# Optimization experiments

Measured on AMD Instinct MI355X. Metric: run time of the kernel, lower is better.

## Reference

```python
import jax, jax.numpy as jnp
import numpy as np

DIM = 512; NHEAD = 8; DHEAD = 64; INNER = NHEAD * DHEAD
CTX = 1024; NOCT = int(np.ceil(np.log2(CTX))) + 1  # 11
B = 8; SEQ = 256; MEM = 768


def positional_encoding(ctx, num_oct):
    # matches Attention.positional_encoding on coords=arange(ctx).view(ctx,1),
    # start_octave = 1 - num_oct
    coords = jnp.arange(ctx, dtype=jnp.float32)[:, None, None]        # (ctx,1,1)
    octaves = jnp.arange(1 - num_oct, 1, dtype=jnp.float32)           # (num_oct,)
    mult = (2.0 ** octaves) * np.pi
    scaled = (coords * mult).reshape(ctx, num_oct)                    # (ctx, num_oct)
    return jnp.concatenate([jnp.sin(scaled), jnp.cos(scaled)], axis=-1)  # (ctx, 2*num_oct)


def get_shifts(mem, seq, ctx):
    coords = jnp.arange(mem + seq - 1, -1, -1) - (seq - 1)            # (mem+seq,)
    shifts = coords[None, :] + jnp.arange(seq)[:, None]               # (seq, mem+seq)
    oob = (shifts < 0) | (shifts > ctx - 1)
    bias = jnp.where(oob, -jnp.inf, 0.0).astype(jnp.float32)
    return jnp.clip(shifts, 0, ctx - 1), bias


def setup_inputs() -> dict:
    key = jax.random.key(0)
    ks = jax.random.split(key, 8)
    s = 0.02
    return {
        "x": jax.random.normal(ks[0], (B, SEQ, DIM), jnp.float32),
        "memory": jax.random.normal(ks[1], (B, MEM, DIM), jnp.float32),
        "W_qkv": jax.random.normal(ks[2], (DIM, 3 * INNER), jnp.float32) * s,
        "W_rel": jax.random.normal(ks[3], (2 * NOCT, INNER), jnp.float32) * s,
        "W_out": jax.random.normal(ks[4], (INNER, DIM), jnp.float32) * s,
        "b_out": jnp.zeros((DIM,), jnp.float32),
        "u_emb": jax.random.normal(ks[5], (DHEAD,), jnp.float32),
        "v_emb": jax.random.normal(ks[6], (DHEAD,), jnp.float32),
    }


def reference(x, memory, W_qkv, W_rel, W_out, b_out, u_emb, v_emb):
    b, seq, _ = x.shape
    mem = memory.shape[1]
    total = mem + seq
    scale = DHEAD ** -0.5

    shifts, bias = get_shifts(mem, seq, CTX)                          # (seq,total) each
    R = positional_encoding(CTX, NOCT)                                # (CTX, 2*NOCT)
    kr = (R @ W_rel)[shifts].reshape(seq, total, NHEAD, DHEAD)        # n m h d

    qkv = jnp.concatenate([memory, x], axis=1) @ W_qkv                # (b,total,3*INNER)
    q, k, v = jnp.split(qkv, 3, axis=-1)

    def heads(t):
        return t.reshape(b, total, NHEAD, DHEAD).transpose(0, 2, 1, 3)  # b h m d

    q = heads(q)[:, :, mem:]                                          # b h n d (queries only over x)
    k = heads(k)
    v = heads(v)

    term_a = jnp.einsum('bhnd,bhmd->bhnm', q, k)
    term_b = jnp.einsum('bhnd,nmhd->bhnm', q, kr)
    term_c = jnp.einsum('d,bhmd->bhm', u_emb, k)[:, :, None, :]        # broadcast over n
    term_d = jnp.einsum('d,nmhd->hnm', v_emb, kr)[None]                # broadcast over b

    dots = (term_a + term_b + term_c + term_d) * scale + bias          # banded -inf mask
    attn = jax.nn.softmax(dots, axis=-1)                               # dropout p=0 -> identity
    out = jnp.einsum('bhnm,bhmd->bnhd', attn, v).reshape(b, seq, INNER)
    return out @ W_out + b_out
```

## Files before the change

### kernel.cpp

```cpp
#include <hip/hip_runtime.h>
#include <hip/hip_bf16.h>
#include <math.h>

typedef unsigned short u16;
typedef unsigned int u32;
typedef __attribute__((ext_vector_type(8))) short short8;
typedef __attribute__((ext_vector_type(4))) float floatx4;

constexpr int kB     = 8;
constexpr int kSEQ   = 256;
constexpr int kMEM   = 768;
constexpr int kTOTAL = 1024;

__device__ __forceinline__ float bf2f(u16 u) {
  return __uint_as_float(((u32)u) << 16);
}
__device__ __forceinline__ u16 f2bf(float f) {
  __hip_bfloat16 h = __float2bfloat16(f);
  return *reinterpret_cast<u16*>(&h);
}
__device__ __forceinline__ void gload_lds16(const u16* g, u16* l) {
  __builtin_amdgcn_global_load_lds(
      (__attribute__((address_space(1))) const unsigned int*)g,
      (__attribute__((address_space(3))) unsigned int*)l, 16, 0, 0);
}

__global__ __launch_bounds__(256) void rrel_kernel(
    const float* __restrict__ W_rel, const float* __restrict__ v_emb,
    u16* __restrict__ Rrel_bf, float* __restrict__ vR)
{
  __shared__ float pe[22];
  __shared__ float prod[512];
  int s = blockIdx.x;
  int t = threadIdx.x;
  if (t < 22) {
    int o = (t < 11) ? t : (t - 11);
    float mult = ldexpf(3.14159265358979323846f, o - 10);
    float ang = (float)s * mult;
    pe[t] = (t < 11) ? sinf(ang) : cosf(ang);
  }
  __syncthreads();
#pragma unroll
  for (int c = 0; c < 2; c++) {
    int j = t + c * 256;
    float acc = 0.f;
#pragma unroll
    for (int o = 0; o < 22; ++o) acc += pe[o] * W_rel[o * 512 + j];
    Rrel_bf[(size_t)s * 512 + j] = f2bf(acc);
    prod[j] = acc * v_emb[j & 63];
  }
  __syncthreads();
  if (t < 8) {
    float a = 0.f;
#pragma unroll 8
    for (int d = 0; d < 64; d++) a += prod[t * 64 + d];
    vR[t * 1024 + s] = a * 0.125f;
  }
}

__device__ __forceinline__ void wtconv_body(
    const float* __restrict__ W, u16* __restrict__ Wt, int K, int N,
    int n0, int k0, int tid, float (*tile)[65])
{
  int r = tid >> 4, c4 = (tid & 15) * 4;
#pragma unroll
  for (int v = 0; v < 4; v++) {
    float4 w4 = *(const float4*)(W + (size_t)(k0 + v * 16 + r) * N + n0 + c4);
    tile[v * 16 + r][c4 + 0] = w4.x;
    tile[v * 16 + r][c4 + 1] = w4.y;
    tile[v * 16 + r][c4 + 2] = w4.z;
    tile[v * 16 + r][c4 + 3] = w4.w;
  }
  __syncthreads();
#pragma unroll
  for (int v = 0; v < 4; v++) {
    int rn = v * 16 + r;
    ushort4 o;
    o.x = f2bf(tile[c4 + 0][rn]);
    o.y = f2bf(tile[c4 + 1][rn]);
    o.z = f2bf(tile[c4 + 2][rn]);
    o.w = f2bf(tile[c4 + 3][rn]);
    *(ushort4*)(Wt + (size_t)(n0 + rn) * K + k0 + c4) = o;
  }
}

__global__ __launch_bounds__(256) void xw_kernel(
    const float* __restrict__ x, const float* __restrict__ memf,
    const float* __restrict__ W_qkv, const float* __restrict__ W_out,
    u16* __restrict__ Xb, u16* __restrict__ WqkvT, u16* __restrict__ WoutT)
{
  __shared__ float tile[64][65];
  int bid = blockIdx.x;
  int tid = threadIdx.x;
  if (bid < 2048) {
    int idx = bid * 256 + tid;
    int row = idx >> 6, c8 = idx & 63;
    int b = row >> 10, pos = row & 1023;
    const float* src = (pos < kMEM)
        ? memf + (size_t)(b * kMEM + pos) * 512
        : x    + (size_t)(b * kSEQ + pos - kMEM) * 512;
    const float4* s4 = (const float4*)(src + c8 * 8);
    float4 a = s4[0], bb = s4[1];
    u16 tmp[8] = {f2bf(a.x),  f2bf(a.y),  f2bf(a.z),  f2bf(a.w),
                  f2bf(bb.x), f2bf(bb.y), f2bf(bb.z), f2bf(bb.w)};
    *(uint4*)(Xb + (size_t)row * 512 + c8 * 8) = *(uint4*)tmp;
  } else if (bid < 2240) {
    int r = bid - 2048;
    wtconv_body(W_qkv, WqkvT, 512, 1536, (r % 24) * 64, (r / 24) * 64, tid, tile);
  } else {
    int r = bid - 2240;
    wtconv_body(W_out, WoutT, 512, 512, (r % 8) * 64, (r / 8) * 64, tid, tile);
  }
}

__global__ __launch_bounds__(256) void gemm_bf16(
    const u16* __restrict__ A, const u16* __restrict__ Bt,
    int lda, int ldb, int ksteps,
    u16* __restrict__ Cbf, float* __restrict__ Cf, int ldc,
    const float* __restrict__ colAdd, int mode)
{
  __shared__ u16 As[128 * 64];
  __shared__ u16 Bs[128 * 64];
  int tid = threadIdx.x;
  int id = blockIdx.y * gridDim.x + blockIdx.x;
  int gy = gridDim.y;
  int bm = (id % gy) * 128, bn = (id / gy) * 128;
  int ln = tid & 15, quad = (tid >> 4) & 3, w = tid >> 6;
  int moff = (w >> 1) * 64, noff = (w & 1) * 64;
  int l7 = ln & 7;
  floatx4 acc[4][4];
#pragma unroll
  for (int mi = 0; mi < 4; mi++)
#pragma unroll
    for (int ni = 0; ni < 4; ni++) acc[mi][ni] = (floatx4){0.f, 0.f, 0.f, 0.f};

  int srow[4], sgch[4];
#pragma unroll
  for (int v = 0; v < 4; v++) {
    int f = v * 256 + tid;
    srow[v] = f >> 3;
    sgch[v] = (f & 7) ^ ((f >> 3) & 7);
  }

  for (int ks = 0; ks < ksteps; ks++) {
    int k0 = ks * 64;
#pragma unroll
    for (int v = 0; v < 4; v++) {
      gload_lds16(A + (size_t)(bm + srow[v]) * lda + k0 + sgch[v] * 8,
                  &As[(v * 256 + tid) * 8]);
      gload_lds16(Bt + (size_t)(bn + srow[v]) * ldb + k0 + sgch[v] * 8,
                  &Bs[(v * 256 + tid) * 8]);
    }
    __syncthreads();
#pragma unroll
    for (int kb = 0; kb < 2; kb++) {
      short8 af[4], bfr[4];
#pragma unroll
      for (int mi = 0; mi < 4; mi++) {
        int row = moff + mi * 16 + ln;
        af[mi] = *(const short8*)&As[row * 64 + (((quad + 4 * kb) ^ l7) << 3)];
      }
#pragma unroll
      for (int ni = 0; ni < 4; ni++) {
        int row = noff + ni * 16 + ln;
        bfr[ni] = *(const short8*)&Bs[row * 64 + (((quad + 4 * kb) ^ l7) << 3)];
      }
#pragma unroll
      for (int mi = 0; mi < 4; mi++)
#pragma unroll
        for (int ni = 0; ni < 4; ni++)
          acc[mi][ni] = __builtin_amdgcn_mfma_f32_16x16x32_bf16(
              af[mi], bfr[ni], acc[mi][ni], 0, 0, 0);
    }
    __syncthreads();
  }

  int r0 = bm + moff + quad * 4;
#pragma unroll
  for (int ni = 0; ni < 4; ni++) {
    int col = bn + noff + ni * 16 + ln;
    float cv = (mode == 2) ? colAdd[col] : 0.f;
    float scale = (mode == 0 && col < 512) ? 0.125f : 1.f;
#pragma unroll
    for (int mi = 0; mi < 4; mi++) {
#pragma unroll
      for (int r = 0; r < 4; r++) {
        int row = r0 + mi * 16 + r;
        float val = acc[mi][ni][r];
        if (mode == 2) Cf[(size_t)row * ldc + col] = val + cv;
        else           Cbf[(size_t)row * ldc + col] = f2bf(val * scale);
      }
    }
  }
}

__global__ __launch_bounds__(256) void uk_kernel(
    const u16* __restrict__ qkv_bf, const float* __restrict__ u_emb,
    float* __restrict__ uk)
{
  int idx = blockIdx.x * 256 + threadIdx.x;
  int b = idx >> 13, h = (idx >> 10) & 7, m = idx & 1023;
  const u16* kp = qkv_bf + (size_t)(b * kTOTAL + m) * 1536 + 512 + h * 64;
  const float4* ue4 = (const float4*)u_emb;
  float acc = 0.f;
#pragma unroll
  for (int c = 0; c < 8; c++) {
    uint4 raw = *(const uint4*)(kp + c * 8);
    const u16* us = (const u16*)&raw;
    float4 ua = ue4[2 * c], ub = ue4[2 * c + 1];
    acc += bf2f(us[0]) * ua.x + bf2f(us[1]) * ua.y + bf2f(us[2]) * ua.z + bf2f(us[3]) * ua.w
         + bf2f(us[4]) * ub.x + bf2f(us[5]) * ub.y + bf2f(us[6]) * ub.z + bf2f(us[7]) * ub.w;
  }
  uk[idx] = acc * 0.125f;
}

__global__ __launch_bounds__(256) void attn_mfma(
    const u16* __restrict__ qkv_bf, const u16* __restrict__ Rrel_bf,
    const float* __restrict__ vR, const float* __restrict__ uk,
    u16* __restrict__ Opart, float* __restrict__ lbuf)
{
  constexpr int LD  = 72;
  constexpr int TLD = 84;
  __shared__ u16 Vt[64 * LD];
  __shared__ u16 Ps[64 * LD];
  __shared__ u16 Tl[4 * 16 * TLD];

  int nt = blockIdx.x >> 3, p = blockIdx.x & 7;
  int h = blockIdx.y, b = blockIdx.z;
  int n0 = nt * 64, bh = b * 8 + h;
  int tid = threadIdx.x;
  int w = tid >> 6, lane = tid & 63;
  int l15 = lane & 15, quad = lane >> 4, q8 = quad * 8;

  int sr0 = tid >> 3, sc8 = tid & 7;
  int sr1 = (256 + tid) >> 3;
  int vg0 = ((sr0 >> 3) ^ sc8) * 8 + (sr0 & 7);
  int vg1 = ((sr1 >> 3) ^ sc8) * 8 + (sr1 & 7);

  const u16* qrow = qkv_bf + (size_t)(b * kTOTAL + kMEM + n0 + 16 * w + l15) * 1536 + h * 64;
  short8 qf0 = *(const short8*)(qrow + q8);
  short8 qf1 = *(const short8*)(qrow + 32 + q8);

  const u16* kpart = qkv_bf + (size_t)(b * kTOTAL) * 1536 + 512 + h * 64;
  const float* ukrow = uk + (size_t)bh * 1024 + l15;
  const float* vRh = vR + h * 1024;
  u16* Tw = Tl + w * 16 * TLD;

  floatx4 o_acc[4];
  float l_i[4];
#pragma unroll
  for (int r = 0; r < 4; r++) l_i[r] = 0.f;
#pragma unroll
  for (int nd = 0; nd < 4; nd++) o_acc[nd] = (floatx4){0.f, 0.f, 0.f, 0.f};

  int s_base_w = kMEM + n0 + 16 * w;
  int ntiles = 13 + nt;
  for (int mt = p; mt < ntiles; mt += 8) {
    int m0 = mt * 64;
    const u16* kbase = kpart + (size_t)m0 * 1536;
    int sb = s_base_w - m0;

    uint4 vreg0 = *(const uint4*)(kbase + 512 + (size_t)sr0 * 1536 + sc8 * 8);
    uint4 vreg1 = *(const uint4*)(kbase + 512 + (size_t)sr1 * 1536 + sc8 * 8);
    short8 kb0[4], kb1[4];
#pragma unroll
    for (int ni = 0; ni < 4; ni++) {
      const u16* kr = kbase + (size_t)(16 * ni + l15) * 1536;
      kb0[ni] = *(const short8*)(kr + q8);
      kb1[ni] = *(const short8*)(kr + 32 + q8);
    }
    short8 rb0[5], rb1[5];
    float vRc[5];
#pragma unroll
    for (int ct = 0; ct < 5; ct++) {
      int s = sb - 63 + 16 * ct + l15;
      s = min(max(s, 0), 1023);
      const u16* rr = Rrel_bf + (size_t)s * 512 + h * 64;
      rb0[ct] = *(const short8*)(rr + q8);
      rb1[ct] = *(const short8*)(rr + 32 + q8);
      vRc[ct] = vRh[s];
    }
    float ukc[4];
#pragma unroll
    for (int ni = 0; ni < 4; ni++) ukc[ni] = ukrow[m0 + ni * 16];

    __syncthreads();
    {
      const u16* vp0 = (const u16*)&vreg0;
      const u16* vp1 = (const u16*)&vreg1;
#pragma unroll
      for (int i = 0; i < 8; i++) {
        Vt[(sc8 * 8 + i) * LD + vg0] = vp0[i];
        Vt[(sc8 * 8 + i) * LD + vg1] = vp1[i];
      }
    }
    __syncthreads();

#pragma unroll
    for (int ct = 0; ct < 5; ct++) {
      floatx4 t = (floatx4){0.f, 0.f, 0.f, 0.f};
      t = __builtin_amdgcn_mfma_f32_16x16x32_bf16(qf0, rb0[ct], t, 0, 0, 0);
      t = __builtin_amdgcn_mfma_f32_16x16x32_bf16(qf1, rb1[ct], t, 0, 0, 0);
#pragma unroll
      for (int r = 0; r < 4; r++)
        Tw[(4 * quad + r) * TLD + 16 * ct + l15] = f2bf(t[r] + vRc[ct]);
    }

    floatx4 s_acc[4];
#pragma unroll
    for (int ni = 0; ni < 4; ni++) {
      floatx4 sa = (floatx4){0.f, 0.f, 0.f, 0.f};
      sa = __builtin_amdgcn_mfma_f32_16x16x32_bf16(qf0, kb0[ni], sa, 0, 0, 0);
      sa = __builtin_amdgcn_mfma_f32_16x16x32_bf16(qf1, kb1[ni], sa, 0, 0, 0);
      s_acc[ni] = sa;
    }

    bool lastt = (mt == ntiles - 1);
#pragma unroll
    for (int r = 0; r < 4; r++) {
      int il = 4 * quad + r;
      float ls = 0.f;
      float pv[4];
#pragma unroll
      for (int ni = 0; ni < 4; ni++) {
        float tsh = bf2f(Tw[il * TLD + 63 + il - 16 * ni - l15]);
        float val = s_acc[ni][r] + tsh + ukc[ni];
        if (lastt && (16 * ni + l15) > (16 * w + il)) val = -1e30f;
        float e = __expf(val);
        pv[ni] = e;
        ls += e;
      }
      l_i[r] += ls;
      int prow = 16 * w + il;
      int rr3p = prow >> 3;
      int base = prow * LD + (l15 & 7);
#pragma unroll
      for (int ni = 0; ni < 4; ni++)
        Ps[base + (((2 * ni + (l15 >> 3)) ^ rr3p) << 3)] = f2bf(pv[ni]);
    }

    int rowq = 16 * w + l15, rr3q = rowq >> 3;
    short8 pa0 = *(const short8*)&Ps[rowq * LD + ((quad ^ rr3q) << 3)];
    short8 pa1 = *(const short8*)&Ps[rowq * LD + (((quad + 4) ^ rr3q) << 3)];
#pragma unroll
    for (int nd = 0; nd < 4; nd++) {
      int rowv = 16 * nd + l15, rr3v = rowv >> 3;
      short8 vb0 = *(const short8*)&Vt[rowv * LD + ((quad ^ rr3v) << 3)];
      short8 vb1 = *(const short8*)&Vt[rowv * LD + (((quad + 4) ^ rr3v) << 3)];
      o_acc[nd] = __builtin_amdgcn_mfma_f32_16x16x32_bf16(pa0, vb0, o_acc[nd], 0, 0, 0);
      o_acc[nd] = __builtin_amdgcn_mfma_f32_16x16x32_bf16(pa1, vb1, o_acc[nd], 0, 0, 0);
    }
  }

  int pbase = (p * 64 + bh) * 256;
#pragma unroll
  for (int r = 0; r < 4; r++) {
    float l = l_i[r];
#pragma unroll
    for (int off = 1; off < 16; off <<= 1)
      l += __shfl_xor(l, off, 64);
    int n = n0 + 16 * w + 4 * quad + r;
    u16* orow = Opart + ((size_t)(pbase + n) << 6) + l15;
#pragma unroll
    for (int nd = 0; nd < 4; nd++)
      orow[16 * nd] = f2bf(o_acc[nd][r]);
    if (l15 == 0) lbuf[pbase + n] = l;
  }
}

__global__ __launch_bounds__(256) void attn_combine(
    const u16* __restrict__ Opart, const float* __restrict__ lbuf,
    u16* __restrict__ aout_bf)
{
  int idx = blockIdx.x * 256 + threadIdx.x;
  int bh = idx >> 12, n = (idx >> 4) & 255, d4 = idx & 15;
  int rowi = bh * 256 + n;
  float den = 0.f;
  float num[4] = {0.f, 0.f, 0.f, 0.f};
#pragma unroll
  for (int p = 0; p < 8; p++) {
    den += lbuf[(p << 14) + rowi];
    uint2 raw = *(const uint2*)(Opart + (((size_t)(p << 14) + rowi) << 6) + d4 * 4);
    const u16* us = (const u16*)&raw;
#pragma unroll
    for (int j = 0; j < 4; j++) num[j] += bf2f(us[j]);
  }
  float inv = 1.f / den;
  int b = bh >> 3, h = bh & 7;
  ushort4 o;
  o.x = f2bf(num[0] * inv);
  o.y = f2bf(num[1] * inv);
  o.z = f2bf(num[2] * inv);
  o.w = f2bf(num[3] * inv);
  *(ushort4*)(aout_bf + (size_t)(b * kSEQ + n) * 512 + h * 64 + d4 * 4) = o;
}

extern "C" void kernel_launch(void* const* d_in, const int* in_sizes, int n_in,
                              void* d_out, int out_size, void* d_ws, size_t ws_size,
                              hipStream_t stream) {
  (void)in_sizes; (void)n_in; (void)out_size; (void)ws_size;
  const float* x      = (const float*)d_in[0];
  const float* memory = (const float*)d_in[1];
  const float* W_qkv  = (const float*)d_in[2];
  const float* W_rel  = (const float*)d_in[3];
  const float* W_out  = (const float*)d_in[4];
  const float* b_out  = (const float*)d_in[5];
  const float* u_emb  = (const float*)d_in[6];
  const float* v_emb  = (const float*)d_in[7];
  float* out = (float*)d_out;

  char* ws = (char*)d_ws;
  u16*   qkv_bf  = (u16*)ws;                         ws += (size_t)12582912 * 2;
  u16*   Xcat_bf = (u16*)ws;                         ws += (size_t)4194304 * 2;
  u16*   aout_bf = (u16*)ws;                         ws += (size_t)1048576 * 2;
  u16*   Opart   = (u16*)ws;                         ws += (size_t)8388608 * 2;
  float* lbuf    = (float*)ws;                       ws += (size_t)131072 * 4;
  u16*   WqkvT   = (u16*)ws;                         ws += (size_t)786432 * 2;
  u16*   WoutT   = (u16*)ws;                         ws += (size_t)262144 * 2;
  u16*   Rrel_bf = (u16*)ws;                         ws += (size_t)524288 * 2;
  float* vR      = (float*)ws;                       ws += (size_t)8192 * 4;
  float* uk      = (float*)ws;                       ws += (size_t)65536 * 4;

  rrel_kernel<<<1024, 256, 0, stream>>>(W_rel, v_emb, Rrel_bf, vR);
  xw_kernel<<<2304, 256, 0, stream>>>(x, memory, W_qkv, W_out, Xcat_bf, WqkvT, WoutT);

  gemm_bf16<<<dim3(12, 64), 256, 0, stream>>>(
      Xcat_bf, WqkvT, 512, 512, 8, qkv_bf, nullptr, 1536, nullptr, 0);

  uk_kernel<<<256, 256, 0, stream>>>(qkv_bf, u_emb, uk);

  attn_mfma<<<dim3(32, 8, 8), 256, 0, stream>>>(qkv_bf, Rrel_bf, vR, uk, Opart, lbuf);
  attn_combine<<<1024, 256, 0, stream>>>(Opart, lbuf, aout_bf);

  gemm_bf16<<<dim3(4, 16), 256, 0, stream>>>(
      aout_bf, WoutT, 512, 512, 8, nullptr, out, 512, b_out, 2);
}
```

Measured before the change: 174.7 us.

## Precompute relative-position bias via batched GEMM and pre-transposed V

Computes the q·R_rel positional term (plus v·R and u·k biases) for every query and relative shift up front with a batched GEMM, scattered into a per-(b,h) skewed bias matrix qB in bf16. A new kernel writes a transposed V copy alongside the u·k reduction. The attention kernel then just reads these bias values and the V^T fragments from global memory, dropping its per-tile R_rel MFMAs, LDS V transpose, skew buffer and two barriers. This adds a large intermediate buffer and extra global traffic, and the bias is now summed before bf16 rounding, which changes numerics slightly.

```diff
diff --git a/kernel.cpp b/kernel.cpp
--- a/kernel.cpp
+++ b/kernel.cpp
@@ -116,12 +116,17 @@
 __global__ __launch_bounds__(256) void gemm_bf16(
     const u16* __restrict__ A, const u16* __restrict__ Bt,
     int lda, int ldb, int ksteps,
-    u16* __restrict__ Cbf, float* __restrict__ Cf, int ldc,
-    const float* __restrict__ colAdd, int mode)
+    long long aStrideB, int aStrideH, int bStrideH,
+    u16* __restrict__ Cbf, float* __restrict__ Cf, int ldc, long long cStrideZ,
+    const float* __restrict__ colAdd, int colAddStrideH,
+    const float* __restrict__ ukp, int mode)
 {
   __shared__ u16 As[128 * 64];
   __shared__ u16 Bs[128 * 64];
   int tid = threadIdx.x;
+  int z = blockIdx.z;
+  const u16* Ab = A + (size_t)(z >> 3) * aStrideB + (size_t)(z & 7) * aStrideH;
+  const u16* Bb = Bt + (size_t)(z & 7) * bStrideH;
   int id = blockIdx.y * gridDim.x + blockIdx.x;
   int gy = gridDim.y;
   int bm = (id % gy) * 128, bn = (id / gy) * 128;
@@ -146,9 +151,9 @@
     int k0 = ks * 64;
 #pragma unroll
     for (int v = 0; v < 4; v++) {
-      gload_lds16(A + (size_t)(bm + srow[v]) * lda + k0 + sgch[v] * 8,
+      gload_lds16(Ab + (size_t)(bm + srow[v]) * lda + k0 + sgch[v] * 8,
                   &As[(v * 256 + tid) * 8]);
-      gload_lds16(Bt + (size_t)(bn + srow[v]) * ldb + k0 + sgch[v] * 8,
+      gload_lds16(Bb + (size_t)(bn + srow[v]) * ldb + k0 + sgch[v] * 8,
                   &Bs[(v * 256 + tid) * 8]);
     }
     __syncthreads();
@@ -176,10 +181,12 @@
   }
 
   int r0 = bm + moff + quad * 4;
+  const float* vRp = (mode == 3) ? colAdd + (size_t)(z & 7) * colAddStrideH : colAdd;
+  const float* ukz = (mode == 3) ? ukp + (size_t)z * 1024 : nullptr;
 #pragma unroll
   for (int ni = 0; ni < 4; ni++) {
     int col = bn + noff + ni * 16 + ln;
-    float cv = (mode == 2) ? colAdd[col] : 0.f;
+    float cv = (mode == 2) ? colAdd[col] : (mode == 3 ? vRp[col] : 0.f);
     float scale = (mode == 0 && col < 512) ? 0.125f : 1.f;
 #pragma unroll
     for (int mi = 0; mi < 4; mi++) {
@@ -187,43 +194,73 @@
       for (int r = 0; r < 4; r++) {
         int row = r0 + mi * 16 + r;
         float val = acc[mi][ni][r];
-        if (mode == 2) Cf[(size_t)row * ldc + col] = val + cv;
-        else           Cbf[(size_t)row * ldc + col] = f2bf(val * scale);
+        if (mode == 2) {
+          Cf[(size_t)row * ldc + col] = val + cv;
+        } else if (mode == 3) {
+          int m = 768 + row - col;
+          if (m >= 0)
+            Cbf[cStrideZ * z + (size_t)row * 1024 + m] = f2bf(val + cv + ukz[m]);
+        } else {
+          Cbf[(size_t)row * ldc + col] = f2bf(val * scale);
+        }
       }
     }
   }
 }
 
-__global__ __launch_bounds__(256) void uk_kernel(
+__global__ __launch_bounds__(256) void ukvt_kernel(
     const u16* __restrict__ qkv_bf, const float* __restrict__ u_emb,
-    float* __restrict__ uk)
-{
-  int idx = blockIdx.x * 256 + threadIdx.x;
-  int b = idx >> 13, h = (idx >> 10) & 7, m = idx & 1023;
-  const u16* kp = qkv_bf + (size_t)(b * kTOTAL + m) * 1536 + 512 + h * 64;
-  const float4* ue4 = (const float4*)u_emb;
-  float acc = 0.f;
-#pragma unroll
-  for (int c = 0; c < 8; c++) {
-    uint4 raw = *(const uint4*)(kp + c * 8);
-    const u16* us = (const u16*)&raw;
-    float4 ua = ue4[2 * c], ub = ue4[2 * c + 1];
-    acc += bf2f(us[0]) * ua.x + bf2f(us[1]) * ua.y + bf2f(us[2]) * ua.z + bf2f(us[3]) * ua.w
-         + bf2f(us[4]) * ub.x + bf2f(us[5]) * ub.y + bf2f(us[6]) * ub.z + bf2f(us[7]) * ub.w;
-  }
-  uk[idx] = acc * 0.125f;
-}
-
-__global__ __launch_bounds__(256) void attn_mfma(
-    const u16* __restrict__ qkv_bf, const u16* __restrict__ Rrel_bf,
-    const float* __restrict__ vR, const float* __restrict__ uk,
-    u16* __restrict__ Opart, float* __restrict__ lbuf)
-{
-  constexpr int LD  = 72;
-  constexpr int TLD = 84;
-  __shared__ u16 Vt[64 * LD];
+    float* __restrict__ uk, u16* __restrict__ VT)
+{
+  __shared__ u16 vt[64 * 72];
+  __shared__ float kred[64 * 8];
+  int bh = blockIdx.x >> 4, mt = blockIdx.x & 15;
+  int b = bh >> 3, h = bh & 7, m0 = mt * 64;
+  int t = threadIdx.x;
+  int c8 = t & 7;
+  const u16* base = qkv_bf + (size_t)(b * kTOTAL + m0) * 1536 + 512 + h * 64 + c8 * 8;
+  float up[8];
+#pragma unroll
+  for (int i = 0; i < 8; i++) up[i] = u_emb[c8 * 8 + i];
+
+#pragma unroll
+  for (int v = 0; v < 2; v++) {
+    int row = (v * 256 + t) >> 3;
+    uint4 kv = *(const uint4*)(base + (size_t)row * 1536);
+    uint4 vv = *(const uint4*)(base + (size_t)row * 1536 + 512);
+    const u16* ku = (const u16*)&kv;
+    const u16* vu = (const u16*)&vv;
+    float s = 0.f;
+#pragma unroll
+    for (int i = 0; i < 8; i++) s += bf2f(ku[i]) * up[i];
+    kred[row * 8 + c8] = s;
+    int vg = (((row >> 3) ^ c8) << 3) + (row & 7);
+#pragma unroll
+    for (int i = 0; i < 8; i++) vt[(c8 * 8 + i) * 72 + vg] = vu[i];
+  }
+  __syncthreads();
+  if (t < 64) {
+    float a = 0.f;
+#pragma unroll
+    for (int i = 0; i < 8; i++) a += kred[t * 8 + i];
+    uk[(size_t)bh * 1024 + m0 + t] = a * 0.125f;
+  }
+#pragma unroll
+  for (int v = 0; v < 2; v++) {
+    int f = v * 256 + t;
+    int d = f >> 3, mc8 = f & 7;
+    uint4 o = *(const uint4*)&vt[d * 72 + (((mc8 ^ (d >> 3)) << 3))];
+    *(uint4*)(VT + ((size_t)(bh * 64 + d) << 10) + m0 + mc8 * 8) = o;
+  }
+}
+
+__global__ __launch_bounds__(256, 4) void attn_mfma(
+    const u16* __restrict__ qkv_bf, const u16* __restrict__ qB,
+    const u16* __restrict__ VT, u16* __restrict__ Opart,
+    float* __restrict__ lbuf)
+{
+  constexpr int LD = 72;
   __shared__ u16 Ps[64 * LD];
-  __shared__ u16 Tl[4 * 16 * TLD];
 
   int nt = blockIdx.x >> 3, p = blockIdx.x & 7;
   int h = blockIdx.y, b = blockIdx.z;
@@ -232,19 +269,13 @@
   int w = tid >> 6, lane = tid & 63;
   int l15 = lane & 15, quad = lane >> 4, q8 = quad * 8;
 
-  int sr0 = tid >> 3, sc8 = tid & 7;
-  int sr1 = (256 + tid) >> 3;
-  int vg0 = ((sr0 >> 3) ^ sc8) * 8 + (sr0 & 7);
-  int vg1 = ((sr1 >> 3) ^ sc8) * 8 + (sr1 & 7);
-
   const u16* qrow = qkv_bf + (size_t)(b * kTOTAL + kMEM + n0 + 16 * w + l15) * 1536 + h * 64;
   short8 qf0 = *(const short8*)(qrow + q8);
   short8 qf1 = *(const short8*)(qrow + 32 + q8);
 
   const u16* kpart = qkv_bf + (size_t)(b * kTOTAL) * 1536 + 512 + h * 64;
-  const float* ukrow = uk + (size_t)bh * 1024 + l15;
-  const float* vRh = vR + h * 1024;
-  u16* Tw = Tl + w * 16 * TLD;
+  const u16* vtbase = VT + ((size_t)(bh * 64) << 10);
+  const u16* qbrow = qB + ((size_t)bh << 18) + (size_t)(n0 + 16 * w + 4 * quad) * 1024 + l15;
 
   floatx4 o_acc[4];
   float l_i[4];
@@ -253,15 +284,11 @@
 #pragma unroll
   for (int nd = 0; nd < 4; nd++) o_acc[nd] = (floatx4){0.f, 0.f, 0.f, 0.f};
 
-  int s_base_w = kMEM + n0 + 16 * w;
   int ntiles = 13 + nt;
   for (int mt = p; mt < ntiles; mt += 8) {
     int m0 = mt * 64;
     const u16* kbase = kpart + (size_t)m0 * 1536;
-    int sb = s_base_w - m0;
-
-    uint4 vreg0 = *(const uint4*)(kbase + 512 + (size_t)sr0 * 1536 + sc8 * 8);
-    uint4 vreg1 = *(const uint4*)(kbase + 512 + (size_t)sr1 * 1536 + sc8 * 8);
+
     short8 kb0[4], kb1[4];
 #pragma unroll
     for (int ni = 0; ni < 4; ni++) {
@@ -269,42 +296,12 @@
       kb0[ni] = *(const short8*)(kr + q8);
       kb1[ni] = *(const short8*)(kr + 32 + q8);
     }
-    short8 rb0[5], rb1[5];
-    float vRc[5];
-#pragma unroll
-    for (int ct = 0; ct < 5; ct++) {
-      int s = sb - 63 + 16 * ct + l15;
-      s = min(max(s, 0), 1023);
-      const u16* rr = Rrel_bf + (size_t)s * 512 + h * 64;
-      rb0[ct] = *(const short8*)(rr + q8);
-      rb1[ct] = *(const short8*)(rr + 32 + q8);
-      vRc[ct] = vRh[s];
-    }
-    float ukc[4];
-#pragma unroll
-    for (int ni = 0; ni < 4; ni++) ukc[ni] = ukrow[m0 + ni * 16];
-
-    __syncthreads();
-    {
-      const u16* vp0 = (const u16*)&vreg0;
-      const u16* vp1 = (const u16*)&vreg1;
-#pragma unroll
-      for (int i = 0; i < 8; i++) {
-        Vt[(sc8 * 8 + i) * LD + vg0] = vp0[i];
-        Vt[(sc8 * 8 + i) * LD + vg1] = vp1[i];
-      }
-    }
-    __syncthreads();
-
-#pragma unroll
-    for (int ct = 0; ct < 5; ct++) {
-      floatx4 t = (floatx4){0.f, 0.f, 0.f, 0.f};
-      t = __builtin_amdgcn_mfma_f32_16x16x32_bf16(qf0, rb0[ct], t, 0, 0, 0);
-      t = __builtin_amdgcn_mfma_f32_16x16x32_bf16(qf1, rb1[ct], t, 0, 0, 0);
+    u16 qbu[4][4];
+#pragma unroll
+    for (int ni = 0; ni < 4; ni++)
 #pragma unroll
       for (int r = 0; r < 4; r++)
-        Tw[(4 * quad + r) * TLD + 16 * ct + l15] = f2bf(t[r] + vRc[ct]);
-    }
+        qbu[ni][r] = qbrow[(size_t)r * 1024 + m0 + 16 * ni];
 
     floatx4 s_acc[4];
 #pragma unroll
@@ -319,24 +316,19 @@
 #pragma unroll
     for (int r = 0; r < 4; r++) {
       int il = 4 * quad + r;
+      int prow = 16 * w + il;
       float ls = 0.f;
-      float pv[4];
+      int rr3p = prow >> 3;
+      int base = prow * LD + (l15 & 7);
 #pragma unroll
       for (int ni = 0; ni < 4; ni++) {
-        float tsh = bf2f(Tw[il * TLD + 63 + il - 16 * ni - l15]);
-        float val = s_acc[ni][r] + tsh + ukc[ni];
-        if (lastt && (16 * ni + l15) > (16 * w + il)) val = -1e30f;
+        float val = s_acc[ni][r] + bf2f(qbu[ni][r]);
+        if (lastt && (16 * ni + l15) > prow) val = -1e30f;
         float e = __expf(val);
-        pv[ni] = e;
         ls += e;
+        Ps[base + (((2 * ni + (l15 >> 3)) ^ rr3p) << 3)] = f2bf(e);
       }
       l_i[r] += ls;
-      int prow = 16 * w + il;
-      int rr3p = prow >> 3;
-      int base = prow * LD + (l15 & 7);
-#pragma unroll
-      for (int ni = 0; ni < 4; ni++)
-        Ps[base + (((2 * ni + (l15 >> 3)) ^ rr3p) << 3)] = f2bf(pv[ni]);
     }
 
     int rowq = 16 * w + l15, rr3q = rowq >> 3;
@@ -344,9 +336,9 @@
     short8 pa1 = *(const short8*)&Ps[rowq * LD + (((quad + 4) ^ rr3q) << 3)];
 #pragma unroll
     for (int nd = 0; nd < 4; nd++) {
-      int rowv = 16 * nd + l15, rr3v = rowv >> 3;
-      short8 vb0 = *(const short8*)&Vt[rowv * LD + ((quad ^ rr3v) << 3)];
-      short8 vb1 = *(const short8*)&Vt[rowv * LD + (((quad + 4) ^ rr3v) << 3)];
+      const u16* vr = vtbase + ((size_t)(16 * nd + l15) << 10) + m0;
+      short8 vb0 = *(const short8*)(vr + q8);
+      short8 vb1 = *(const short8*)(vr + 32 + q8);
       o_acc[nd] = __builtin_amdgcn_mfma_f32_16x16x32_bf16(pa0, vb0, o_acc[nd], 0, 0, 0);
       o_acc[nd] = __builtin_amdgcn_mfma_f32_16x16x32_bf16(pa1, vb1, o_acc[nd], 0, 0, 0);
     }
@@ -412,6 +404,8 @@
   char* ws = (char*)d_ws;
   u16*   qkv_bf  = (u16*)ws;                         ws += (size_t)12582912 * 2;
   u16*   Xcat_bf = (u16*)ws;                         ws += (size_t)4194304 * 2;
+  u16*   qB      = (u16*)ws;                         ws += (size_t)16777216 * 2;
+  u16*   VT      = (u16*)ws;                         ws += (size_t)4194304 * 2;
   u16*   aout_bf = (u16*)ws;                         ws += (size_t)1048576 * 2;
   u16*   Opart   = (u16*)ws;                         ws += (size_t)8388608 * 2;
   float* lbuf    = (float*)ws;                       ws += (size_t)131072 * 4;
@@ -424,14 +418,21 @@
   rrel_kernel<<<1024, 256, 0, stream>>>(W_rel, v_emb, Rrel_bf, vR);
   xw_kernel<<<2304, 256, 0, stream>>>(x, memory, W_qkv, W_out, Xcat_bf, WqkvT, WoutT);
 
-  gemm_bf16<<<dim3(12, 64), 256, 0, stream>>>(
-      Xcat_bf, WqkvT, 512, 512, 8, qkv_bf, nullptr, 1536, nullptr, 0);
-
-  uk_kernel<<<256, 256, 0, stream>>>(qkv_bf, u_emb, uk);
-
-  attn_mfma<<<dim3(32, 8, 8), 256, 0, stream>>>(qkv_bf, Rrel_bf, vR, uk, Opart, lbuf);
+  gemm_bf16<<<dim3(12, 64, 1), 256, 0, stream>>>(
+      Xcat_bf, WqkvT, 512, 512, 8, 0, 0, 0,
+      qkv_bf, nullptr, 1536, 0, nullptr, 0, nullptr, 0);
+
+  ukvt_kernel<<<1024, 256, 0, stream>>>(qkv_bf, u_emb, uk, VT);
+
+  gemm_bf16<<<dim3(8, 2, 64), 256, 0, stream>>>(
+      qkv_bf + (size_t)768 * 1536, Rrel_bf, 1536, 512, 1,
+      (long long)1024 * 1536, 64, 64,
+      qB, nullptr, 1024, 262144, vR, 1024, uk, 3);
+
+  attn_mfma<<<dim3(32, 8, 8), 256, 0, stream>>>(qkv_bf, qB, VT, Opart, lbuf);
   attn_combine<<<1024, 256, 0, stream>>>(Opart, lbuf, aout_bf);
 
-  gemm_bf16<<<dim3(4, 16), 256, 0, stream>>>(
-      aout_bf, WoutT, 512, 512, 8, nullptr, out, 512, b_out, 2);
-}
+  gemm_bf16<<<dim3(4, 16, 1), 256, 0, stream>>>(
+      aout_bf, WoutT, 512, 512, 8, 0, 0, 0,
+      nullptr, out, 512, 0, b_out, 0, nullptr, 2);
+}
```

New measurement: 203.8 us. 16.6% more time.

## Precompute relative-position scores with batched GEMM before attention

Applied to the files above, without the earlier changes.

Moves the q·R relative-position term (plus the v·R bias) out of the attention kernel into a separate batched bf16 GEMM. Each batch-head computes Q times all 1024 relative embeddings and scatters the result into a shifted (query, key) score buffer. The attention kernel then reads one precomputed bf16 value per score element instead of running extra MFMAs and an LDS shift per tile. In exchange it adds a 32 MB intermediate buffer that must be written and read back, which trades compute and LDS traffic for global memory bandwidth. The extra launch computes all 1024 relative positions, including ones the band later discards.

```diff
diff --git a/kernel.cpp b/kernel.cpp
--- a/kernel.cpp
+++ b/kernel.cpp
@@ -116,12 +116,16 @@
 __global__ __launch_bounds__(256) void gemm_bf16(
     const u16* __restrict__ A, const u16* __restrict__ Bt,
     int lda, int ldb, int ksteps,
-    u16* __restrict__ Cbf, float* __restrict__ Cf, int ldc,
-    const float* __restrict__ colAdd, int mode)
+    long long aStrideB, int aStrideH, int bStrideH,
+    u16* __restrict__ Cbf, float* __restrict__ Cf, int ldc, long long cStrideZ,
+    const float* __restrict__ colAdd, int colAddStrideH, int mode)
 {
   __shared__ u16 As[128 * 64];
   __shared__ u16 Bs[128 * 64];
   int tid = threadIdx.x;
+  int z = blockIdx.z;
+  const u16* Ab = A + (size_t)(z >> 3) * aStrideB + (size_t)(z & 7) * aStrideH;
+  const u16* Bb = Bt + (size_t)(z & 7) * bStrideH;
   int id = blockIdx.y * gridDim.x + blockIdx.x;
   int gy = gridDim.y;
   int bm = (id % gy) * 128, bn = (id / gy) * 128;
@@ -146,9 +150,9 @@
     int k0 = ks * 64;
 #pragma unroll
     for (int v = 0; v < 4; v++) {
-      gload_lds16(A + (size_t)(bm + srow[v]) * lda + k0 + sgch[v] * 8,
+      gload_lds16(Ab + (size_t)(bm + srow[v]) * lda + k0 + sgch[v] * 8,
                   &As[(v * 256 + tid) * 8]);
-      gload_lds16(Bt + (size_t)(bn + srow[v]) * ldb + k0 + sgch[v] * 8,
+      gload_lds16(Bb + (size_t)(bn + srow[v]) * ldb + k0 + sgch[v] * 8,
                   &Bs[(v * 256 + tid) * 8]);
     }
     __syncthreads();
@@ -176,10 +180,11 @@
   }
 
   int r0 = bm + moff + quad * 4;
+  const float* vRp = (mode == 3) ? colAdd + (size_t)(z & 7) * colAddStrideH : colAdd;
 #pragma unroll
   for (int ni = 0; ni < 4; ni++) {
     int col = bn + noff + ni * 16 + ln;
-    float cv = (mode == 2) ? colAdd[col] : 0.f;
+    float cv = (mode == 2) ? colAdd[col] : (mode == 3 ? vRp[col] : 0.f);
     float scale = (mode == 0 && col < 512) ? 0.125f : 1.f;
 #pragma unroll
     for (int mi = 0; mi < 4; mi++) {
@@ -187,8 +192,15 @@
       for (int r = 0; r < 4; r++) {
         int row = r0 + mi * 16 + r;
         float val = acc[mi][ni][r];
-        if (mode == 2) Cf[(size_t)row * ldc + col] = val + cv;
-        else           Cbf[(size_t)row * ldc + col] = f2bf(val * scale);
+        if (mode == 2) {
+          Cf[(size_t)row * ldc + col] = val + cv;
+        } else if (mode == 3) {
+          int m = 768 + row - col;
+          if (m >= 0)
+            Cbf[cStrideZ * z + (size_t)row * 1024 + m] = f2bf(val + cv);
+        } else {
+          Cbf[(size_t)row * ldc + col] = f2bf(val * scale);
+        }
       }
     }
   }
@@ -215,15 +227,13 @@
 }
 
 __global__ __launch_bounds__(256) void attn_mfma(
-    const u16* __restrict__ qkv_bf, const u16* __restrict__ Rrel_bf,
-    const float* __restrict__ vR, const float* __restrict__ uk,
-    u16* __restrict__ Opart, float* __restrict__ lbuf)
-{
-  constexpr int LD  = 72;
-  constexpr int TLD = 84;
+    const u16* __restrict__ qkv_bf, const u16* __restrict__ qB,
+    const float* __restrict__ uk, u16* __restrict__ Opart,
+    float* __restrict__ lbuf)
+{
+  constexpr int LD = 72;
   __shared__ u16 Vt[64 * LD];
   __shared__ u16 Ps[64 * LD];
-  __shared__ u16 Tl[4 * 16 * TLD];
 
   int nt = blockIdx.x >> 3, p = blockIdx.x & 7;
   int h = blockIdx.y, b = blockIdx.z;
@@ -242,9 +252,8 @@
   short8 qf1 = *(const short8*)(qrow + 32 + q8);
 
   const u16* kpart = qkv_bf + (size_t)(b * kTOTAL) * 1536 + 512 + h * 64;
+  const u16* qbrow = qB + ((size_t)bh << 18) + (size_t)(n0 + 16 * w + 4 * quad) * 1024 + l15;
   const float* ukrow = uk + (size_t)bh * 1024 + l15;
-  const float* vRh = vR + h * 1024;
-  u16* Tw = Tl + w * 16 * TLD;
 
   floatx4 o_acc[4];
   float l_i[4];
@@ -253,12 +262,10 @@
 #pragma unroll
   for (int nd = 0; nd < 4; nd++) o_acc[nd] = (floatx4){0.f, 0.f, 0.f, 0.f};
 
-  int s_base_w = kMEM + n0 + 16 * w;
   int ntiles = 13 + nt;
   for (int mt = p; mt < ntiles; mt += 8) {
     int m0 = mt * 64;
     const u16* kbase = kpart + (size_t)m0 * 1536;
-    int sb = s_base_w - m0;
 
     uint4 vreg0 = *(const uint4*)(kbase + 512 + (size_t)sr0 * 1536 + sc8 * 8);
     uint4 vreg1 = *(const uint4*)(kbase + 512 + (size_t)sr1 * 1536 + sc8 * 8);
@@ -269,20 +276,15 @@
       kb0[ni] = *(const short8*)(kr + q8);
       kb1[ni] = *(const short8*)(kr + 32 + q8);
     }
-    short8 rb0[5], rb1[5];
-    float vRc[5];
-#pragma unroll
-    for (int ct = 0; ct < 5; ct++) {
-      int s = sb - 63 + 16 * ct + l15;
-      s = min(max(s, 0), 1023);
-      const u16* rr = Rrel_bf + (size_t)s * 512 + h * 64;
-      rb0[ct] = *(const short8*)(rr + q8);
-      rb1[ct] = *(const short8*)(rr + 32 + q8);
-      vRc[ct] = vRh[s];
-    }
+    u16 qbu[4][4];
+#pragma unroll
+    for (int ni = 0; ni < 4; ni++)
+#pragma unroll
+      for (int r = 0; r < 4; r++)
+        qbu[ni][r] = qbrow[(size_t)r * 1024 + m0 + 16 * ni];
     float ukc[4];
 #pragma unroll
-    for (int ni = 0; ni < 4; ni++) ukc[ni] = ukrow[m0 + ni * 16];
+    for (int ni = 0; ni < 4; ni++) ukc[ni] = ukrow[m0 + 16 * ni];
 
     __syncthreads();
     {
@@ -295,16 +297,6 @@
       }
     }
     __syncthreads();
-
-#pragma unroll
-    for (int ct = 0; ct < 5; ct++) {
-      floatx4 t = (floatx4){0.f, 0.f, 0.f, 0.f};
-      t = __builtin_amdgcn_mfma_f32_16x16x32_bf16(qf0, rb0[ct], t, 0, 0, 0);
-      t = __builtin_amdgcn_mfma_f32_16x16x32_bf16(qf1, rb1[ct], t, 0, 0, 0);
-#pragma unroll
-      for (int r = 0; r < 4; r++)
-        Tw[(4 * quad + r) * TLD + 16 * ct + l15] = f2bf(t[r] + vRc[ct]);
-    }
 
     floatx4 s_acc[4];
 #pragma unroll
@@ -319,24 +311,19 @@
 #pragma unroll
     for (int r = 0; r < 4; r++) {
       int il = 4 * quad + r;
+      int prow = 16 * w + il;
       float ls = 0.f;
-      float pv[4];
+      int rr3p = prow >> 3;
+      int base = prow * LD + (l15 & 7);
 #pragma unroll
       for (int ni = 0; ni < 4; ni++) {
-        float tsh = bf2f(Tw[il * TLD + 63 + il - 16 * ni - l15]);
-        float val = s_acc[ni][r] + tsh + ukc[ni];
-        if (lastt && (16 * ni + l15) > (16 * w + il)) val = -1e30f;
+        float val = s_acc[ni][r] + bf2f(qbu[ni][r]) + ukc[ni];
+        if (lastt && (16 * ni + l15) > prow) val = -1e30f;
         float e = __expf(val);
-        pv[ni] = e;
         ls += e;
+        Ps[base + (((2 * ni + (l15 >> 3)) ^ rr3p) << 3)] = f2bf(e);
       }
       l_i[r] += ls;
-      int prow = 16 * w + il;
-      int rr3p = prow >> 3;
-      int base = prow * LD + (l15 & 7);
-#pragma unroll
-      for (int ni = 0; ni < 4; ni++)
-        Ps[base + (((2 * ni + (l15 >> 3)) ^ rr3p) << 3)] = f2bf(pv[ni]);
     }
 
     int rowq = 16 * w + l15, rr3q = rowq >> 3;
@@ -412,6 +399,7 @@
   char* ws = (char*)d_ws;
   u16*   qkv_bf  = (u16*)ws;                         ws += (size_t)12582912 * 2;
   u16*   Xcat_bf = (u16*)ws;                         ws += (size_t)4194304 * 2;
+  u16*   qB      = (u16*)ws;                         ws += (size_t)16777216 * 2;
   u16*   aout_bf = (u16*)ws;                         ws += (size_t)1048576 * 2;
   u16*   Opart   = (u16*)ws;                         ws += (size_t)8388608 * 2;
   float* lbuf    = (float*)ws;                       ws += (size_t)131072 * 4;
@@ -424,14 +412,21 @@
   rrel_kernel<<<1024, 256, 0, stream>>>(W_rel, v_emb, Rrel_bf, vR);
   xw_kernel<<<2304, 256, 0, stream>>>(x, memory, W_qkv, W_out, Xcat_bf, WqkvT, WoutT);
 
-  gemm_bf16<<<dim3(12, 64), 256, 0, stream>>>(
-      Xcat_bf, WqkvT, 512, 512, 8, qkv_bf, nullptr, 1536, nullptr, 0);
+  gemm_bf16<<<dim3(12, 64, 1), 256, 0, stream>>>(
+      Xcat_bf, WqkvT, 512, 512, 8, 0, 0, 0,
+      qkv_bf, nullptr, 1536, 0, nullptr, 0, 0);
 
   uk_kernel<<<256, 256, 0, stream>>>(qkv_bf, u_emb, uk);
 
-  attn_mfma<<<dim3(32, 8, 8), 256, 0, stream>>>(qkv_bf, Rrel_bf, vR, uk, Opart, lbuf);
+  gemm_bf16<<<dim3(8, 2, 64), 256, 0, stream>>>(
+      qkv_bf + (size_t)768 * 1536, Rrel_bf, 1536, 512, 1,
+      (long long)1024 * 1536, 64, 64,
+      qB, nullptr, 1024, 262144, vR, 1024, 3);
+
+  attn_mfma<<<dim3(32, 8, 8), 256, 0, stream>>>(qkv_bf, qB, uk, Opart, lbuf);
   attn_combine<<<1024, 256, 0, stream>>>(Opart, lbuf, aout_bf);
 
-  gemm_bf16<<<dim3(4, 16), 256, 0, stream>>>(
-      aout_bf, WoutT, 512, 512, 8, nullptr, out, 512, b_out, 2);
-}
+  gemm_bf16<<<dim3(4, 16, 1), 256, 0, stream>>>(
+      aout_bf, WoutT, 512, 512, 8, 0, 0, 0,
+      nullptr, out, 512, 0, b_out, 0, 2);
+}
```

New measurement: 189.6 us. 1.09x slower.
